# Performance work log

Measured on AMD Instinct MI355X. Metric: run time of the kernel, lower is better.

## Reference

```python
import jax, jax.numpy as jnp
import numpy as np

# TT factorization of a 4096 -> 4096 linear layer
IN_SHAPE = (8, 8, 8, 8)    # input_tt_shape, prod = 4096
OUT_SHAPE = (8, 8, 8, 8)   # output_tt_shape, prod = 4096
RANKS = (1, 16, 16, 16, 1) # tt_ranks, len = n_dim + 1
N_DIM = len(IN_SHAPE)
BATCH = 2048
OUT_SIZE = int(np.prod(OUT_SHAPE))
IN_SIZE = int(np.prod(IN_SHAPE))


def setup_inputs() -> dict:
    key = jax.random.key(0)
    ks = jax.random.split(key, N_DIM + 1)
    x = jax.random.normal(ks[0], (BATCH, IN_SIZE), dtype=jnp.float32)
    inp = {"x": x}
    for i in range(N_DIM):
        rows = RANKS[i] * OUT_SHAPE[i]
        cols = IN_SHAPE[i] * RANKS[i + 1]
        # xavier_uniform scale, matching torch init statistics
        limit = float(np.sqrt(6.0 / (rows + cols)))
        inp[f"core{i}"] = jax.random.uniform(
            ks[i + 1], (rows, cols), minval=-limit, maxval=limit, dtype=jnp.float32
        )
    inp["bias"] = jnp.zeros((OUT_SIZE,), dtype=jnp.float32)
    return inp


def reference(x, core0, core1, core2, core3, bias):
    cores = [core0, core1, core2, core3]
    res = x  # [B, prod(IN_SHAPE)]
    # Sequential TT-core contraction, last mode first (faithful to torch loop)
    for k in range(N_DIM - 1, -1, -1):
        res = res.reshape(-1, IN_SHAPE[k])                     # [.., n_k]
        res = res.T                                            # [n_k, ..]
        res = res.reshape(RANKS[k + 1] * IN_SHAPE[k], -1)      # [r_{k+1}*n_k, ..]
        res = cores[k] @ res                                   # [r_k*m_k, ..]
    res = res.reshape(OUT_SIZE, -1).T                          # [B, prod(OUT_SHAPE)]
    return res + bias
```

## Files before the change

### kernel.cpp

```cpp
#include <hip/hip_runtime.h>
#include <hip/hip_bf16.h>
#include <stdint.h>


typedef __bf16 bf16_t;
typedef __bf16 bf16x8 __attribute__((ext_vector_type(8)));
typedef __bf16 bf16x4 __attribute__((ext_vector_type(4)));
typedef float floatx4 __attribute__((ext_vector_type(4)));

#define BATCH_N 2048
#define KD 4096
#define ND 4096

__device__ static inline void load_lds16(const void* g, void* l) {
    __builtin_amdgcn_global_load_lds(
        (const __attribute__((address_space(1))) void*)g,
        (__attribute__((address_space(3))) void*)l, 16, 0, 0);
}

__global__ __launch_bounds__(256) void prep0(const float* __restrict__ x,
                                             const float* __restrict__ c0,
                                             const float* __restrict__ c1,
                                             const float* __restrict__ c2,
                                             const float* __restrict__ c3,
                                             bf16_t* __restrict__ xb,
                                             float* __restrict__ Pg,
                                             float* __restrict__ Tg) {
    const int t = threadIdx.x;
    const int b = blockIdx.x;

    if (b < 4096) {
        int g = b * 256 + t;
        const float4* xv = (const float4*)x;
        float4 a = xv[g * 2];
        float4 c = xv[g * 2 + 1];
        bf16x8 o;
        o[0] = (bf16_t)a.x; o[1] = (bf16_t)a.y; o[2] = (bf16_t)a.z; o[3] = (bf16_t)a.w;
        o[4] = (bf16_t)c.x; o[5] = (bf16_t)c.y; o[6] = (bf16_t)c.z; o[7] = (bf16_t)c.w;
        ((bf16x8*)xb)[g] = o;
        return;
    }

    __shared__ float s0[128];
    __shared__ float s1[2048];

    if (b < 4160) {
        const int n01 = b - 4096, n0 = n01 >> 3, n1 = n01 & 7;
        if (t < 128) s0[t] = c0[(t >> 4) * 128 + n0 * 16 + (t & 15)];
        for (int i = t; i < 2048; i += 256) {
            int r1 = i >> 7, m1 = (i >> 4) & 7, r2 = i & 15;
            s1[i] = c1[(r1 * 8 + m1) * 128 + n1 * 16 + r2];
        }
        __syncthreads();
#pragma unroll
        for (int j = 0; j < 4; ++j) {
            int o = j * 256 + t, m01 = o >> 4, r2 = o & 15;
            int m0 = m01 >> 3, m1 = m01 & 7;
            float s = 0.f;
#pragma unroll
            for (int r1 = 0; r1 < 16; ++r1)
                s += s0[m0 * 16 + r1] * s1[r1 * 128 + m1 * 16 + r2];
            Pg[n01 * 1024 + o] = s;
        }
        return;
    }

    {
        const int m23 = b - 4160, m2 = m23 >> 3, m3 = m23 & 7;
        if (t < 128) s0[t] = c3[((t >> 3) * 8 + m3) * 8 + (t & 7)];
        for (int i = t; i < 2048; i += 256) {
            int r2 = i >> 7, n2 = (i >> 4) & 7, r3 = i & 15;
            s1[i] = c2[(r2 * 8 + m2) * 128 + n2 * 16 + r3];
        }
        __syncthreads();
#pragma unroll
        for (int j = 0; j < 4; ++j) {
            int o = j * 256 + t, n23 = o >> 4, r2 = o & 15;
            int n2 = n23 >> 3, n3 = n23 & 7;
            float s = 0.f;
#pragma unroll
            for (int r3 = 0; r3 < 16; ++r3)
                s += s1[r2 * 128 + n2 * 16 + r3] * s0[r3 * 8 + n3];
            Tg[m23 * 1024 + o] = s;
        }
    }
}

__global__ __launch_bounds__(256) void build_w(const float* __restrict__ Pg,
                                               const float* __restrict__ Tg,
                                               bf16_t* __restrict__ W) {
    const int t = threadIdx.x;
    const int b = blockIdx.x;
    const int n01 = b & 63, q = b >> 6;
    const int cg = t & 15;
    const int mr = t >> 4;
    const float* Pb = Pg + n01 * 1024 + q * 256;

#pragma unroll 1
    for (int ms = 0; ms < 4; ++ms) {
        const int m23 = ms * 16 + mr;
        float Tr[4][16];
#pragma unroll
        for (int jj = 0; jj < 4; ++jj) {
            const float4* tp = (const float4*)(Tg + (m23 * 64 + cg * 4 + jj) * 16);
#pragma unroll
            for (int w = 0; w < 4; ++w) {
                float4 v = tp[w];
                Tr[jj][w * 4 + 0] = v.x;
                Tr[jj][w * 4 + 1] = v.y;
                Tr[jj][w * 4 + 2] = v.z;
                Tr[jj][w * 4 + 3] = v.w;
            }
        }
#pragma unroll 4
        for (int ml = 0; ml < 16; ++ml) {
            float a0 = 0.f, a1 = 0.f, a2 = 0.f, a3 = 0.f;
#pragma unroll
            for (int r2 = 0; r2 < 16; ++r2) {
                float p = Pb[ml * 16 + r2];
                a0 += p * Tr[0][r2];
                a1 += p * Tr[1][r2];
                a2 += p * Tr[2][r2];
                a3 += p * Tr[3][r2];
            }
            bf16x4 o;
            o[0] = (bf16_t)a0; o[1] = (bf16_t)a1; o[2] = (bf16_t)a2; o[3] = (bf16_t)a3;
            *(bf16x4*)(W + (size_t)((q * 16 + ml) * 64 + m23) * 4096 + n01 * 64 + cg * 4) = o;
        }
    }
}

__global__ __launch_bounds__(512, 2) void gemm_bt2(const bf16_t* __restrict__ A,
                                                   const bf16_t* __restrict__ B,
                                                   const float* __restrict__ bias,
                                                   float* __restrict__ C) {
    __shared__ bf16_t smem[3][24576];
    const int t = threadIdx.x;
    const int bid = blockIdx.x;
    const int xcd = bid & 7, i = bid >> 3;
    const int bm = (xcd & 1) * 8 + (i & 7);
    const int bn = (xcd >> 1) * 4 + (i >> 3);
    const int lane = t & 63, wave = t >> 6;
    const int wm = wave >> 2, wn = wave & 3;

    const int srow = t >> 3;
    const int lc = (t & 7) ^ (srow & 7);
    const bf16_t* Ag = A + (size_t)(bm * 128 + srow) * KD + lc * 8;
    const bf16_t* Bg = B + (size_t)(bn * 256 + srow) * KD + lc * 8;
    const int woff = wave * 512;

    floatx4 acc[4][4];
    floatx4 zero = {0.f, 0.f, 0.f, 0.f};
#pragma unroll
    for (int i2 = 0; i2 < 4; ++i2)
#pragma unroll
        for (int j = 0; j < 4; ++j) acc[i2][j] = zero;

    const int fr = lane & 15;
    const int fc = lane >> 4;

#pragma unroll
    for (int kt = 0; kt < 2; ++kt) {
        bf16_t* bb = &smem[kt][0];
        const size_t ko = (size_t)kt * 64;
#pragma unroll
        for (int c = 0; c < 2; ++c)
            load_lds16(Ag + (size_t)c * 64 * KD + ko, bb + c * 4096 + woff);
#pragma unroll
        for (int c = 0; c < 4; ++c)
            load_lds16(Bg + (size_t)c * 64 * KD + ko, bb + 8192 + c * 4096 + woff);
    }
    asm volatile("s_waitcnt vmcnt(6)\n\ts_barrier" ::: "memory");

    int cur = 0;
#pragma unroll 1
    for (int kt = 0; kt < 64; ++kt) {
        if (kt < 62) {
            int nb = cur + 2; if (nb >= 3) nb -= 3;
            bf16_t* bb = &smem[nb][0];
            const size_t ko = (size_t)(kt + 2) * 64;
#pragma unroll
            for (int c = 0; c < 2; ++c)
                load_lds16(Ag + (size_t)c * 64 * KD + ko, bb + c * 4096 + woff);
#pragma unroll
            for (int c = 0; c < 4; ++c)
                load_lds16(Bg + (size_t)c * 64 * KD + ko, bb + 8192 + c * 4096 + woff);
        }

        const bf16_t* Ab = &smem[cur][0];
        const bf16_t* Bb = &smem[cur][8192];
#pragma unroll
        for (int kk = 0; kk < 2; ++kk) {
            const int pA = (fc + kk * 4) ^ (fr & 7);
            bf16x8 af[4], bf[4];
#pragma unroll
            for (int im = 0; im < 4; ++im)
                af[im] = *(const bf16x8*)(Ab + (wm * 64 + im * 16 + fr) * 64 + pA * 8);
#pragma unroll
            for (int in = 0; in < 4; ++in)
                bf[in] = *(const bf16x8*)(Bb + (wn * 64 + in * 16 + fr) * 64 + pA * 8);
            __builtin_amdgcn_s_setprio(1);
#pragma unroll
            for (int im = 0; im < 4; ++im)
#pragma unroll
                for (int in = 0; in < 4; ++in)
                    acc[im][in] = __builtin_amdgcn_mfma_f32_16x16x32_bf16(
                        af[im], bf[in], acc[im][in], 0, 0, 0);
            __builtin_amdgcn_s_setprio(0);
        }

        if (kt < 62) {
            asm volatile("s_waitcnt vmcnt(6) lgkmcnt(0)\n\ts_barrier" ::: "memory");
        } else if (kt == 62) {
            asm volatile("s_waitcnt vmcnt(0) lgkmcnt(0)\n\ts_barrier" ::: "memory");
        }
        cur = (cur == 2) ? 0 : cur + 1;
    }

    const int rl = lane >> 4, cl = lane & 15;
    const size_t rbase = (size_t)bm * 128 + wm * 64;
    const int cbase = bn * 256 + wn * 64;
#pragma unroll
    for (int im = 0; im < 4; ++im) {
#pragma unroll
        for (int in = 0; in < 4; ++in) {
            int col = cbase + in * 16 + cl;
            float bv = bias[col];
#pragma unroll
            for (int r = 0; r < 4; ++r) {
                size_t row = rbase + im * 16 + rl * 4 + r;
                C[row * ND + col] = acc[im][in][r] + bv;
            }
        }
    }
}

extern "C" void kernel_launch(void* const* d_in, const int* in_sizes, int n_in,
                              void* d_out, int out_size, void* d_ws, size_t ws_size,
                              hipStream_t stream) {
    const float* x  = (const float*)d_in[0];
    const float* c0 = (const float*)d_in[1];
    const float* c1 = (const float*)d_in[2];
    const float* c2 = (const float*)d_in[3];
    const float* c3 = (const float*)d_in[4];
    const float* bias = (const float*)d_in[5];
    float* out = (float*)d_out;

    char* ws = (char*)d_ws;
    bf16_t* Xb = (bf16_t*)ws;
    bf16_t* W  = (bf16_t*)(ws + (16u << 20));

    float* Pg = (float*)d_out;
    float* Tg = Pg + 64 * 1024;

    prep0<<<4224, 256, 0, stream>>>(x, c0, c1, c2, c3, Xb, Pg, Tg);
    build_w<<<256, 256, 0, stream>>>(Pg, Tg, W);
    gemm_bt2<<<256, 512, 0, stream>>>(Xb, W, bias, out);
}
```

Baseline: 171.8 us.

## Retile GEMM to 128x128 blocks with 256 threads and 32-wide K steps

The bf16 GEMM moves from 128x256 tiles with 512 threads and K=64 stages to 128x128 tiles with 256 threads, K=32 stages and 512 blocks. The LDS layout is redone so each 64-element row holds two paired matrix rows, with a new swizzle for the fragment reads. The triple-buffer footprint shrinks so three blocks can share a CU, aiming for better occupancy and a fuller grid. In exchange, each output element needs more global loads and the kernel runs twice as many barriers per K.

```diff
diff --git a/kernel.cpp b/kernel.cpp
--- a/kernel.cpp
+++ b/kernel.cpp
@@ -130,23 +130,23 @@
     }
 }
 
-__global__ __launch_bounds__(512, 2) void gemm_bt2(const bf16_t* __restrict__ A,
+__global__ __launch_bounds__(256, 3) void gemm_bt4(const bf16_t* __restrict__ A,
                                                    const bf16_t* __restrict__ B,
                                                    const float* __restrict__ bias,
                                                    float* __restrict__ C) {
-    __shared__ bf16_t smem[3][24576];
+    __shared__ bf16_t smem[3][8192];
     const int t = threadIdx.x;
     const int bid = blockIdx.x;
     const int xcd = bid & 7, i = bid >> 3;
     const int bm = (xcd & 1) * 8 + (i & 7);
-    const int bn = (xcd >> 1) * 4 + (i >> 3);
+    const int bn = (xcd >> 1) * 8 + (i >> 3);
     const int lane = t & 63, wave = t >> 6;
-    const int wm = wave >> 2, wn = wave & 3;
-
-    const int srow = t >> 3;
-    const int lc = (t & 7) ^ (srow & 7);
-    const bf16_t* Ag = A + (size_t)(bm * 128 + srow) * KD + lc * 8;
-    const bf16_t* Bg = B + (size_t)(bn * 256 + srow) * KD + lc * 8;
+    const int wm = wave >> 1, wn = wave & 1;
+
+    const int cl = (t & 7) ^ ((t >> 3) & 7);
+    const int fp = cl >> 2, fkc = cl & 3;
+    const bf16_t* Ag = A + (size_t)(bm * 128 + 2 * (t >> 3) + fp) * KD + fkc * 8;
+    const bf16_t* Bg = B + (size_t)(bn * 128 + 2 * (t >> 3) + fp) * KD + fkc * 8;
     const int woff = wave * 512;
 
     floatx4 acc[4][4];
@@ -158,73 +158,69 @@
 
     const int fr = lane & 15;
     const int fc = lane >> 4;
+    const int fr2 = fr >> 1;
+    const int chOff = ((((fr & 1) << 2) | fc) ^ fr2) * 8;
 
 #pragma unroll
     for (int kt = 0; kt < 2; ++kt) {
         bf16_t* bb = &smem[kt][0];
-        const size_t ko = (size_t)kt * 64;
-#pragma unroll
-        for (int c = 0; c < 2; ++c)
-            load_lds16(Ag + (size_t)c * 64 * KD + ko, bb + c * 4096 + woff);
-#pragma unroll
-        for (int c = 0; c < 4; ++c)
-            load_lds16(Bg + (size_t)c * 64 * KD + ko, bb + 8192 + c * 4096 + woff);
-    }
-    asm volatile("s_waitcnt vmcnt(6)\n\ts_barrier" ::: "memory");
+        const size_t ko = (size_t)kt * 32;
+#pragma unroll
+        for (int c = 0; c < 2; ++c) {
+            load_lds16(Ag + (size_t)c * 64 * KD + ko, bb + c * 2048 + woff);
+            load_lds16(Bg + (size_t)c * 64 * KD + ko, bb + 4096 + c * 2048 + woff);
+        }
+    }
+    asm volatile("s_waitcnt vmcnt(4)\n\ts_barrier" ::: "memory");
 
     int cur = 0;
 #pragma unroll 1
-    for (int kt = 0; kt < 64; ++kt) {
-        if (kt < 62) {
+    for (int kt = 0; kt < 128; ++kt) {
+        if (kt < 126) {
             int nb = cur + 2; if (nb >= 3) nb -= 3;
             bf16_t* bb = &smem[nb][0];
-            const size_t ko = (size_t)(kt + 2) * 64;
-#pragma unroll
-            for (int c = 0; c < 2; ++c)
-                load_lds16(Ag + (size_t)c * 64 * KD + ko, bb + c * 4096 + woff);
-#pragma unroll
-            for (int c = 0; c < 4; ++c)
-                load_lds16(Bg + (size_t)c * 64 * KD + ko, bb + 8192 + c * 4096 + woff);
+            const size_t ko = (size_t)(kt + 2) * 32;
+#pragma unroll
+            for (int c = 0; c < 2; ++c) {
+                load_lds16(Ag + (size_t)c * 64 * KD + ko, bb + c * 2048 + woff);
+                load_lds16(Bg + (size_t)c * 64 * KD + ko, bb + 4096 + c * 2048 + woff);
+            }
         }
 
         const bf16_t* Ab = &smem[cur][0];
-        const bf16_t* Bb = &smem[cur][8192];
-#pragma unroll
-        for (int kk = 0; kk < 2; ++kk) {
-            const int pA = (fc + kk * 4) ^ (fr & 7);
-            bf16x8 af[4], bf[4];
-#pragma unroll
-            for (int im = 0; im < 4; ++im)
-                af[im] = *(const bf16x8*)(Ab + (wm * 64 + im * 16 + fr) * 64 + pA * 8);
+        const bf16_t* Bb = &smem[cur][4096];
+        bf16x8 af[4], bf[4];
+#pragma unroll
+        for (int im = 0; im < 4; ++im)
+            af[im] = *(const bf16x8*)(Ab + (wm * 32 + im * 8 + fr2) * 64 + chOff);
+#pragma unroll
+        for (int in = 0; in < 4; ++in)
+            bf[in] = *(const bf16x8*)(Bb + (wn * 32 + in * 8 + fr2) * 64 + chOff);
+        __builtin_amdgcn_s_setprio(1);
+#pragma unroll
+        for (int im = 0; im < 4; ++im)
 #pragma unroll
             for (int in = 0; in < 4; ++in)
-                bf[in] = *(const bf16x8*)(Bb + (wn * 64 + in * 16 + fr) * 64 + pA * 8);
-            __builtin_amdgcn_s_setprio(1);
-#pragma unroll
-            for (int im = 0; im < 4; ++im)
-#pragma unroll
-                for (int in = 0; in < 4; ++in)
-                    acc[im][in] = __builtin_amdgcn_mfma_f32_16x16x32_bf16(
-                        af[im], bf[in], acc[im][in], 0, 0, 0);
-            __builtin_amdgcn_s_setprio(0);
-        }
-
-        if (kt < 62) {
-            asm volatile("s_waitcnt vmcnt(6) lgkmcnt(0)\n\ts_barrier" ::: "memory");
-        } else if (kt == 62) {
+                acc[im][in] = __builtin_amdgcn_mfma_f32_16x16x32_bf16(
+                    af[im], bf[in], acc[im][in], 0, 0, 0);
+        __builtin_amdgcn_s_setprio(0);
+
+        if (kt < 126) {
+            asm volatile("s_waitcnt vmcnt(4) lgkmcnt(0)\n\ts_barrier" ::: "memory");
+        } else if (kt == 126) {
             asm volatile("s_waitcnt vmcnt(0) lgkmcnt(0)\n\ts_barrier" ::: "memory");
         }
         cur = (cur == 2) ? 0 : cur + 1;
     }
 
-    const int rl = lane >> 4, cl = lane & 15;
+    const int rl = lane >> 4, cl2 = lane & 15;
     const size_t rbase = (size_t)bm * 128 + wm * 64;
-    const int cbase = bn * 256 + wn * 64;
+    const int cbase = bn * 128 + wn * 64;
 #pragma unroll
     for (int im = 0; im < 4; ++im) {
 #pragma unroll
         for (int in = 0; in < 4; ++in) {
-            int col = cbase + in * 16 + cl;
+            int col = cbase + in * 16 + cl2;
             float bv = bias[col];
 #pragma unroll
             for (int r = 0; r < 4; ++r) {
@@ -255,5 +251,5 @@
 
     prep0<<<4224, 256, 0, stream>>>(x, c0, c1, c2, c3, Xb, Pg, Tg);
     build_w<<<256, 256, 0, stream>>>(Pg, Tg, W);
-    gemm_bt2<<<256, 512, 0, stream>>>(Xb, W, bias, out);
-}
+    gemm_bt4<<<512, 256, 0, stream>>>(Xb, W, bias, out);
+}
```

Measured after the change: 183.8 us. +7.0%, slower.

## Load A fragments directly from global into registers, stage only B in LDS

Applied to the files above, without the earlier changes.

The GEMM now reads the A operand straight from global memory into double-banked register fragments instead of staging it through LDS, and keeps only B in a smaller triple-buffered LDS ring. The loop is unrolled by two so the register banks alternate, with vmcnt waits tuned for the new outstanding-load counts. This cuts LDS traffic, LDS footprint and ds_read work per step. In exchange it adds register pressure and uncoalesced global loads for A, and several waves re-read the same A rows.

```diff
diff --git a/kernel.cpp b/kernel.cpp
--- a/kernel.cpp
+++ b/kernel.cpp
@@ -130,25 +130,28 @@
     }
 }
 
-__global__ __launch_bounds__(512, 2) void gemm_bt2(const bf16_t* __restrict__ A,
+__global__ __launch_bounds__(512, 2) void gemm_bt6(const bf16_t* __restrict__ A,
                                                    const bf16_t* __restrict__ B,
                                                    const float* __restrict__ bias,
                                                    float* __restrict__ C) {
-    __shared__ bf16_t smem[3][24576];
+    __shared__ bf16_t smem[3][16384];
     const int t = threadIdx.x;
     const int bid = blockIdx.x;
-    const int xcd = bid & 7, i = bid >> 3;
-    const int bm = (xcd & 1) * 8 + (i & 7);
-    const int bn = (xcd >> 1) * 4 + (i >> 3);
+    const int xcd = bid & 7, gi = bid >> 3;
+    const int bm = (xcd & 1) * 8 + (gi & 7);
+    const int bn = (xcd >> 1) * 4 + (gi >> 3);
     const int lane = t & 63, wave = t >> 6;
     const int wm = wave >> 2, wn = wave & 3;
 
     const int srow = t >> 3;
     const int lc = (t & 7) ^ (srow & 7);
-    const bf16_t* Ag = A + (size_t)(bm * 128 + srow) * KD + lc * 8;
     const bf16_t* Bg = B + (size_t)(bn * 256 + srow) * KD + lc * 8;
     const int woff = wave * 512;
 
+    const int fr = lane & 15;
+    const int fc = lane >> 4;
+    const bf16_t* Aptr = A + (size_t)(bm * 128 + wm * 64 + fr) * KD + fc * 8;
+
     floatx4 acc[4][4];
     floatx4 zero = {0.f, 0.f, 0.f, 0.f};
 #pragma unroll
@@ -156,66 +159,95 @@
 #pragma unroll
         for (int j = 0; j < 4; ++j) acc[i2][j] = zero;
 
-    const int fr = lane & 15;
-    const int fc = lane >> 4;
-
-#pragma unroll
-    for (int kt = 0; kt < 2; ++kt) {
-        bf16_t* bb = &smem[kt][0];
-        const size_t ko = (size_t)kt * 64;
-#pragma unroll
-        for (int c = 0; c < 2; ++c)
-            load_lds16(Ag + (size_t)c * 64 * KD + ko, bb + c * 4096 + woff);
-#pragma unroll
-        for (int c = 0; c < 4; ++c)
-            load_lds16(Bg + (size_t)c * 64 * KD + ko, bb + 8192 + c * 4096 + woff);
-    }
-    asm volatile("s_waitcnt vmcnt(6)\n\ts_barrier" ::: "memory");
+    bf16x8 afA[8], afB[8];
+
+#define LOADA(bank, kt)                                                        \
+    {                                                                          \
+        _Pragma("unroll")                                                      \
+        for (int im = 0; im < 4; ++im) {                                       \
+            _Pragma("unroll")                                                  \
+            for (int kk = 0; kk < 2; ++kk)                                     \
+                bank[im * 2 + kk] = *(const bf16x8*)(                          \
+                    Aptr + (size_t)(im * 16) * KD + (kt) * 64 + kk * 32);      \
+        }                                                                      \
+    }
+
+#define STAGEB(kt, buf)                                                        \
+    {                                                                          \
+        bf16_t* bb = &smem[buf][0];                                            \
+        const size_t ko = (size_t)(kt) * 64;                                   \
+        _Pragma("unroll")                                                      \
+        for (int c = 0; c < 4; ++c)                                            \
+            load_lds16(Bg + (size_t)c * 64 * KD + ko, bb + c * 4096 + woff);   \
+    }
+
+#define COMPUTE(bank, cur)                                                     \
+    {                                                                          \
+        const bf16_t* Bb = &smem[cur][0];                                      \
+        _Pragma("unroll")                                                      \
+        for (int kk = 0; kk < 2; ++kk) {                                       \
+            const int pA = (fc + kk * 4) ^ (fr & 7);                           \
+            bf16x8 bf[4];                                                      \
+            _Pragma("unroll")                                                  \
+            for (int in = 0; in < 4; ++in)                                     \
+                bf[in] = *(const bf16x8*)(Bb + (wn * 64 + in * 16 + fr) * 64 + \
+                                          pA * 8);                             \
+            __builtin_amdgcn_s_setprio(1);                                     \
+            _Pragma("unroll")                                                  \
+            for (int im = 0; im < 4; ++im) {                                   \
+                _Pragma("unroll")                                              \
+                for (int in = 0; in < 4; ++in)                                 \
+                    acc[im][in] = __builtin_amdgcn_mfma_f32_16x16x32_bf16(     \
+                        bank[im * 2 + kk], bf[in], acc[im][in], 0, 0, 0);      \
+            }                                                                  \
+            __builtin_amdgcn_s_setprio(0);                                     \
+        }                                                                      \
+    }
+
+    STAGEB(0, 0);
+    STAGEB(1, 1);
+    LOADA(afA, 0);
+    asm volatile("s_waitcnt vmcnt(0)\n\ts_barrier" ::: "memory");
 
     int cur = 0;
 #pragma unroll 1
-    for (int kt = 0; kt < 64; ++kt) {
-        if (kt < 62) {
-            int nb = cur + 2; if (nb >= 3) nb -= 3;
-            bf16_t* bb = &smem[nb][0];
-            const size_t ko = (size_t)(kt + 2) * 64;
-#pragma unroll
-            for (int c = 0; c < 2; ++c)
-                load_lds16(Ag + (size_t)c * 64 * KD + ko, bb + c * 4096 + woff);
-#pragma unroll
-            for (int c = 0; c < 4; ++c)
-                load_lds16(Bg + (size_t)c * 64 * KD + ko, bb + 8192 + c * 4096 + woff);
-        }
-
-        const bf16_t* Ab = &smem[cur][0];
-        const bf16_t* Bb = &smem[cur][8192];
-#pragma unroll
-        for (int kk = 0; kk < 2; ++kk) {
-            const int pA = (fc + kk * 4) ^ (fr & 7);
-            bf16x8 af[4], bf[4];
-#pragma unroll
-            for (int im = 0; im < 4; ++im)
-                af[im] = *(const bf16x8*)(Ab + (wm * 64 + im * 16 + fr) * 64 + pA * 8);
-#pragma unroll
-            for (int in = 0; in < 4; ++in)
-                bf[in] = *(const bf16x8*)(Bb + (wn * 64 + in * 16 + fr) * 64 + pA * 8);
-            __builtin_amdgcn_s_setprio(1);
-#pragma unroll
-            for (int im = 0; im < 4; ++im)
-#pragma unroll
-                for (int in = 0; in < 4; ++in)
-                    acc[im][in] = __builtin_amdgcn_mfma_f32_16x16x32_bf16(
-                        af[im], bf[in], acc[im][in], 0, 0, 0);
-            __builtin_amdgcn_s_setprio(0);
-        }
-
-        if (kt < 62) {
-            asm volatile("s_waitcnt vmcnt(6) lgkmcnt(0)\n\ts_barrier" ::: "memory");
-        } else if (kt == 62) {
-            asm volatile("s_waitcnt vmcnt(0) lgkmcnt(0)\n\ts_barrier" ::: "memory");
-        }
-        cur = (cur == 2) ? 0 : cur + 1;
-    }
+    for (int j = 0; j < 32; ++j) {
+        const int kt0 = 2 * j;
+        {
+            if (kt0 < 62) {
+                int nb = cur + 2; if (nb >= 3) nb -= 3;
+                STAGEB(kt0 + 2, nb);
+            }
+            LOADA(afB, kt0 + 1);
+            if (j < 31) {
+                asm volatile("s_waitcnt vmcnt(12)" ::: "memory");
+            } else {
+                asm volatile("s_waitcnt vmcnt(8)" ::: "memory");
+            }
+            COMPUTE(afA, cur);
+            asm volatile("s_waitcnt lgkmcnt(0)\n\ts_barrier" ::: "memory");
+            cur = (cur == 2) ? 0 : cur + 1;
+        }
+        {
+            const int kt1 = kt0 + 1;
+            if (kt1 < 62) {
+                int nb = cur + 2; if (nb >= 3) nb -= 3;
+                STAGEB(kt1 + 2, nb);
+            }
+            if (kt1 < 63) LOADA(afA, kt1 + 1);
+            if (j < 31) {
+                asm volatile("s_waitcnt vmcnt(12)" ::: "memory");
+            } else {
+                asm volatile("s_waitcnt vmcnt(0)" ::: "memory");
+            }
+            COMPUTE(afB, cur);
+            asm volatile("s_waitcnt lgkmcnt(0)\n\ts_barrier" ::: "memory");
+            cur = (cur == 2) ? 0 : cur + 1;
+        }
+    }
+#undef LOADA
+#undef STAGEB
+#undef COMPUTE
 
     const int rl = lane >> 4, cl = lane & 15;
     const size_t rbase = (size_t)bm * 128 + wm * 64;
@@ -255,5 +287,5 @@
 
     prep0<<<4224, 256, 0, stream>>>(x, c0, c1, c2, c3, Xb, Pg, Tg);
     build_w<<<256, 256, 0, stream>>>(Pg, Tg, W);
-    gemm_bt2<<<256, 512, 0, stream>>>(Xb, W, bias, out);
-}
+    gemm_bt6<<<256, 512, 0, stream>>>(Xb, W, bias, out);
+}
```

Result: slower. 262.6 us (+52.9%).
